# Kernel optimization log

Hardware: AMD Instinct MI355X
Metric: run time of the kernel (lower is better)

## Reference

```python
import jax, jax.numpy as jnp
import numpy as np

HIDDEN_DIM = 512
N = 2 * HIDDEN_DIM  # 1024
B, T_K = 32, 2048


def setup_inputs() -> dict:
    key = jax.random.key(0)
    ks = jax.random.split(key, 10)
    s_t_hat = jax.random.normal(ks[0], (B, N), dtype=jnp.float32)
    encoder_outputs = jax.random.normal(ks[1], (B, T_K, N), dtype=jnp.float32)
    encoder_feature = jax.random.normal(ks[2], (B * T_K, N), dtype=jnp.float32)
    stmt_feature = jax.random.uniform(ks[3], (B, T_K), dtype=jnp.float32) * 0.01
    enc_padding_mask = jnp.ones((B, T_K), dtype=jnp.float32)
    coverage = jax.random.uniform(ks[4], (B, T_K), dtype=jnp.float32)
    # learned params
    W_dec = jax.random.normal(ks[5], (N, N), dtype=jnp.float32) / np.sqrt(N)
    b_dec = jnp.zeros((N,), dtype=jnp.float32)
    v_w = jax.random.normal(ks[6], (N,), dtype=jnp.float32) / np.sqrt(N)
    W_c = jax.random.normal(ks[7], (N,), dtype=jnp.float32)  # Linear(1, N, bias=False)
    return {
        "s_t_hat": s_t_hat,
        "encoder_outputs": encoder_outputs,
        "encoder_feature": encoder_feature,
        "stmt_feature": stmt_feature,
        "enc_padding_mask": enc_padding_mask,
        "coverage": coverage,
        "W_dec": W_dec,
        "b_dec": b_dec,
        "v_w": v_w,
        "W_c": W_c,
    }


def reference(s_t_hat, encoder_outputs, encoder_feature, stmt_feature,
              enc_padding_mask, coverage, W_dec, b_dec, v_w, W_c):
    b, t_k, n = encoder_outputs.shape
    # decode_proj: [b, n]
    dec_fea = s_t_hat @ W_dec.T + b_dec
    # broadcast-add decoder feature + coverage feature (Linear(1, n) == outer product)
    att_features = (encoder_feature.reshape(b, t_k, n)
                    + dec_fea[:, None, :]
                    + coverage[:, :, None] * W_c)  # [b, t_k, n]
    e = jnp.tanh(att_features)
    scores = jnp.einsum('btn,n->bt', e, v_w)  # v: Linear(n, 1, bias=False)
    attn_dist_ = jax.nn.softmax(scores, axis=1) * enc_padding_mask
    attn_dist = attn_dist_ / attn_dist_.sum(axis=1, keepdims=True)
    attn_dist = attn_dist + stmt_feature * enc_padding_mask
    c_t = jnp.einsum('bt,btn->bn', attn_dist, encoder_outputs)  # bmm
    coverage_out = coverage + attn_dist
    return (c_t, attn_dist, coverage_out)
```

## Files before the change

### kernel.cpp

```cpp
#include <hip/hip_runtime.h>

#define B   32
#define TK  2048
#define N   1024
#define NF4 256

#define OUT_CT   0
#define OUT_ATTN (B * N)
#define OUT_COV  (B * N + B * TK)

#define NSLICE 32
#define TPS    (TK / NSLICE)

typedef float v4f __attribute__((ext_vector_type(4)));

__device__ __forceinline__ float hw_exp2(float x) {
    return __builtin_amdgcn_exp2f(x);
}

__device__ __forceinline__ float fast_tanh(float x) {
    float t = hw_exp2(x * 2.8853900817779268f);
    return 1.0f - 2.0f * __builtin_amdgcn_rcpf(t + 1.0f);
}

__device__ __forceinline__ float wave_reduce_sum(float v) {
#pragma unroll
    for (int off = 32; off > 0; off >>= 1) v += __shfl_xor(v, off, 64);
    return v;
}

__device__ __forceinline__ float4 ldnt(const float4* p) {
    v4f v = __builtin_nontemporal_load((const v4f*)p);
    return make_float4(v.x, v.y, v.z, v.w);
}

__global__ __launch_bounds__(256) void decfea_kernel(
    const float4* __restrict__ S,
    const float4* __restrict__ W,
    const float*  __restrict__ bias,
    float*        __restrict__ dec)
{
    int w    = blockIdx.x * 4 + (threadIdx.x >> 6);
    int lane = threadIdx.x & 63;
    int n    = w >> 3;
    int b0   = (w & 7) * 4;

    float4 wr[4];
#pragma unroll
    for (int j = 0; j < 4; ++j) wr[j] = W[n * NF4 + j * 64 + lane];

#pragma unroll
    for (int i = 0; i < 4; ++i) {
        int b = b0 + i;
        float acc = 0.0f;
#pragma unroll
        for (int j = 0; j < 4; ++j) {
            float4 s4 = S[b * NF4 + j * 64 + lane];
            acc += s4.x * wr[j].x + s4.y * wr[j].y + s4.z * wr[j].z + s4.w * wr[j].w;
        }
        acc = wave_reduce_sum(acc);
        if (lane == 0) dec[b * N + n] = acc + bias[n];
    }
}

__global__ __launch_bounds__(256) void scores_kernel(
    const float4* __restrict__ EF,
    const float4* __restrict__ DEC,
    const float4* __restrict__ WC,
    const float4* __restrict__ VW,
    const float*  __restrict__ cov,
    float*        __restrict__ scores)
{
    int w    = blockIdx.x * 4 + (threadIdx.x >> 6);
    int lane = threadIdx.x & 63;
    int r0   = w * 2;
    int b    = r0 >> 11;
    float c0 = cov[r0];
    float c1 = cov[r0 + 1];

    const float4* ef0 = EF + (size_t)r0 * NF4;
    const float4* ef1 = ef0 + NF4;
    const float4* de  = DEC + b * NF4;

    float p0 = 0.0f, p1 = 0.0f;
#pragma unroll
    for (int j = 0; j < 4; ++j) {
        int f = j * 64 + lane;
        float4 e0 = ldnt(ef0 + f);
        float4 e1 = ldnt(ef1 + f);
        float4 d  = de[f];
        float4 wc = WC[f];
        float4 vw = VW[f];
        p0 += fast_tanh(e0.x + d.x + c0 * wc.x) * vw.x;
        p0 += fast_tanh(e0.y + d.y + c0 * wc.y) * vw.y;
        p0 += fast_tanh(e0.z + d.z + c0 * wc.z) * vw.z;
        p0 += fast_tanh(e0.w + d.w + c0 * wc.w) * vw.w;
        p1 += fast_tanh(e1.x + d.x + c1 * wc.x) * vw.x;
        p1 += fast_tanh(e1.y + d.y + c1 * wc.y) * vw.y;
        p1 += fast_tanh(e1.z + d.z + c1 * wc.z) * vw.z;
        p1 += fast_tanh(e1.w + d.w + c1 * wc.w) * vw.w;
    }
    p0 = wave_reduce_sum(p0);
    p1 = wave_reduce_sum(p1);
    if (lane == 0) {
        scores[r0]     = p0;
        scores[r0 + 1] = p1;
    }
}

__global__ __launch_bounds__(256) void softmax_kernel(
    const float* __restrict__ scores,
    const float* __restrict__ mask,
    const float* __restrict__ stmt,
    const float* __restrict__ coverage,
    float*       __restrict__ out)
{
    int b = blockIdx.x, tid = threadIdx.x;
    __shared__ float red[256];

    float s[8];
    float m = -1e30f;
#pragma unroll
    for (int k = 0; k < 8; ++k) {
        s[k] = scores[b * TK + k * 256 + tid];
        m = fmaxf(m, s[k]);
    }
    red[tid] = m;
    __syncthreads();
    for (int step = 128; step > 0; step >>= 1) {
        if (tid < step) red[tid] = fmaxf(red[tid], red[tid + step]);
        __syncthreads();
    }
    float M = red[0];
    __syncthreads();

    float e[8];
    float loc = 0.0f;
#pragma unroll
    for (int k = 0; k < 8; ++k) {
        int t = k * 256 + tid;
        e[k] = hw_exp2((s[k] - M) * 1.4426950408889634f) * mask[b * TK + t];
        loc += e[k];
    }
    red[tid] = loc;
    __syncthreads();
    for (int step = 128; step > 0; step >>= 1) {
        if (tid < step) red[tid] += red[tid + step];
        __syncthreads();
    }
    float inv = 1.0f / red[0];

#pragma unroll
    for (int k = 0; k < 8; ++k) {
        int t = k * 256 + tid;
        int r = b * TK + t;
        float a = e[k] * inv + stmt[r] * mask[r];
        out[OUT_ATTN + r] = a;
        out[OUT_COV + r]  = coverage[r] + a;
    }
}

__global__ __launch_bounds__(256) void ct_partial_kernel(
    const float4* __restrict__ EO,
    const float*  __restrict__ attn,
    float4*       __restrict__ part)
{
    int s = blockIdx.x;
    int b = blockIdx.y;
    int tid = threadIdx.x;

    __shared__ float wbuf[TPS];
    if (tid < TPS) wbuf[tid] = attn[b * TK + s * TPS + tid];
    __syncthreads();

    float4 acc = {0.0f, 0.0f, 0.0f, 0.0f};
    const float4* eo = EO + ((size_t)b * TK + s * TPS) * NF4 + tid;
#pragma unroll 8
    for (int tt = 0; tt < TPS; ++tt) {
        float w  = wbuf[tt];
        float4 v = ldnt(eo + (size_t)tt * NF4);
        acc.x += w * v.x;
        acc.y += w * v.y;
        acc.z += w * v.z;
        acc.w += w * v.w;
    }
    part[((size_t)s * B + b) * NF4 + tid] = acc;
}

__global__ __launch_bounds__(256) void ct_reduce_kernel(
    const float4* __restrict__ part,
    float4*       __restrict__ ct)
{
    int i = blockIdx.x * 256 + threadIdx.x;
    float4 acc = {0.0f, 0.0f, 0.0f, 0.0f};
#pragma unroll
    for (int s = 0; s < NSLICE; ++s) {
        float4 v = part[(size_t)s * (B * NF4) + i];
        acc.x += v.x;
        acc.y += v.y;
        acc.z += v.z;
        acc.w += v.w;
    }
    ct[i] = acc;
}

extern "C" void kernel_launch(void* const* d_in, const int* in_sizes, int n_in,
                              void* d_out, int out_size, void* d_ws, size_t ws_size,
                              hipStream_t stream) {
    const float* s_t_hat = (const float*)d_in[0];
    const float* EO      = (const float*)d_in[1];
    const float* EF      = (const float*)d_in[2];
    const float* stmt    = (const float*)d_in[3];
    const float* mask    = (const float*)d_in[4];
    const float* cov     = (const float*)d_in[5];
    const float* Wdec    = (const float*)d_in[6];
    const float* bdec    = (const float*)d_in[7];
    const float* vw      = (const float*)d_in[8];
    const float* wc      = (const float*)d_in[9];

    float* out = (float*)d_out;
    float* ws  = (float*)d_ws;
    float* dec    = ws;
    float* scores = ws + B * N;
    float* part   = ws + B * N + B * TK;

    decfea_kernel<<<2048, 256, 0, stream>>>(
        (const float4*)s_t_hat, (const float4*)Wdec, bdec, dec);

    scores_kernel<<<8192, 256, 0, stream>>>(
        (const float4*)EF, (const float4*)dec, (const float4*)wc,
        (const float4*)vw, cov, scores);

    softmax_kernel<<<B, 256, 0, stream>>>(scores, mask, stmt, cov, out);

    ct_partial_kernel<<<dim3(NSLICE, B), 256, 0, stream>>>(
        (const float4*)EO, out + OUT_ATTN, (float4*)part);

    ct_reduce_kernel<<<32, 256, 0, stream>>>(
        (const float4*)part, (float4*)(out + OUT_CT));
}
```

Measured before the change: 506.5 us.

## Fuse softmax into context kernel, split c_t by feature slice, widen scores rows

Removes the separate softmax and c_t reduce kernels. Each context block now recomputes the per-batch softmax redundantly and owns a 32-float feature slice across all 2048 timesteps, reducing within the block through shared memory instead of writing and re-reading a partial-sum buffer. The scores kernel now processes four rows per wave instead of two. The trade-offs are that softmax work is repeated 32 times per batch, and encoder_outputs reads are now short strided 128-byte segments per row rather than full contiguous rows.

After: 518.2 us. +2.3%, slower.

```diff
diff --git a/kernel.cpp b/kernel.cpp
--- a/kernel.cpp
+++ b/kernel.cpp
@@ -9,8 +9,8 @@
 #define OUT_ATTN (B * N)
 #define OUT_COV  (B * N + B * TK)
 
-#define NSLICE 32
-#define TPS    (TK / NSLICE)
+#define NS   32
+#define SF4  (NF4 / NS)
 
 typedef float v4f __attribute__((ext_vector_type(4)));
 
@@ -73,21 +73,21 @@
 {
     int w    = blockIdx.x * 4 + (threadIdx.x >> 6);
     int lane = threadIdx.x & 63;
-    int r0   = w * 2;
+    int r0   = w * 4;
     int b    = r0 >> 11;
-    float c0 = cov[r0];
-    float c1 = cov[r0 + 1];
-
-    const float4* ef0 = EF + (size_t)r0 * NF4;
-    const float4* ef1 = ef0 + NF4;
-    const float4* de  = DEC + b * NF4;
-
-    float p0 = 0.0f, p1 = 0.0f;
+    float c0 = cov[r0], c1 = cov[r0 + 1], c2 = cov[r0 + 2], c3 = cov[r0 + 3];
+
+    const float4* ef = EF + (size_t)r0 * NF4;
+    const float4* de = DEC + b * NF4;
+
+    float p0 = 0.0f, p1 = 0.0f, p2 = 0.0f, p3 = 0.0f;
 #pragma unroll
     for (int j = 0; j < 4; ++j) {
         int f = j * 64 + lane;
-        float4 e0 = ldnt(ef0 + f);
-        float4 e1 = ldnt(ef1 + f);
+        float4 e0 = ldnt(ef + f);
+        float4 e1 = ldnt(ef + NF4 + f);
+        float4 e2 = ldnt(ef + 2 * NF4 + f);
+        float4 e3 = ldnt(ef + 3 * NF4 + f);
         float4 d  = de[f];
         float4 wc = WC[f];
         float4 vw = VW[f];
@@ -99,31 +99,45 @@
         p1 += fast_tanh(e1.y + d.y + c1 * wc.y) * vw.y;
         p1 += fast_tanh(e1.z + d.z + c1 * wc.z) * vw.z;
         p1 += fast_tanh(e1.w + d.w + c1 * wc.w) * vw.w;
+        p2 += fast_tanh(e2.x + d.x + c2 * wc.x) * vw.x;
+        p2 += fast_tanh(e2.y + d.y + c2 * wc.y) * vw.y;
+        p2 += fast_tanh(e2.z + d.z + c2 * wc.z) * vw.z;
+        p2 += fast_tanh(e2.w + d.w + c2 * wc.w) * vw.w;
+        p3 += fast_tanh(e3.x + d.x + c3 * wc.x) * vw.x;
+        p3 += fast_tanh(e3.y + d.y + c3 * wc.y) * vw.y;
+        p3 += fast_tanh(e3.z + d.z + c3 * wc.z) * vw.z;
+        p3 += fast_tanh(e3.w + d.w + c3 * wc.w) * vw.w;
     }
     p0 = wave_reduce_sum(p0);
     p1 = wave_reduce_sum(p1);
+    p2 = wave_reduce_sum(p2);
+    p3 = wave_reduce_sum(p3);
     if (lane == 0) {
-        scores[r0]     = p0;
-        scores[r0 + 1] = p1;
-    }
-}
-
-__global__ __launch_bounds__(256) void softmax_kernel(
-    const float* __restrict__ scores,
-    const float* __restrict__ mask,
-    const float* __restrict__ stmt,
-    const float* __restrict__ coverage,
-    float*       __restrict__ out)
+        *(float4*)(scores + r0) = make_float4(p0, p1, p2, p3);
+    }
+}
+
+__global__ __launch_bounds__(256) void ct_fused_kernel(
+    const float4* __restrict__ EO,
+    const float*  __restrict__ scores,
+    const float*  __restrict__ mask,
+    const float*  __restrict__ stmt,
+    const float*  __restrict__ coverage,
+    float*        __restrict__ out)
 {
-    int b = blockIdx.x, tid = threadIdx.x;
+    int s   = blockIdx.x;
+    int b   = blockIdx.y;
+    int tid = threadIdx.x;
+
+    __shared__ __align__(16) float attn_s[TK];
     __shared__ float red[256];
 
-    float s[8];
+    float sc[8];
     float m = -1e30f;
 #pragma unroll
     for (int k = 0; k < 8; ++k) {
-        s[k] = scores[b * TK + k * 256 + tid];
-        m = fmaxf(m, s[k]);
+        sc[k] = scores[b * TK + k * 256 + tid];
+        m = fmaxf(m, sc[k]);
     }
     red[tid] = m;
     __syncthreads();
@@ -139,7 +153,7 @@
 #pragma unroll
     for (int k = 0; k < 8; ++k) {
         int t = k * 256 + tid;
-        e[k] = hw_exp2((s[k] - M) * 1.4426950408889634f) * mask[b * TK + t];
+        e[k] = hw_exp2((sc[k] - M) * 1.4426950408889634f) * mask[b * TK + t];
         loc += e[k];
     }
     red[tid] = loc;
@@ -155,53 +169,41 @@
         int t = k * 256 + tid;
         int r = b * TK + t;
         float a = e[k] * inv + stmt[r] * mask[r];
-        out[OUT_ATTN + r] = a;
-        out[OUT_COV + r]  = coverage[r] + a;
-    }
-}
-
-__global__ __launch_bounds__(256) void ct_partial_kernel(
-    const float4* __restrict__ EO,
-    const float*  __restrict__ attn,
-    float4*       __restrict__ part)
-{
-    int s = blockIdx.x;
-    int b = blockIdx.y;
-    int tid = threadIdx.x;
-
-    __shared__ float wbuf[TPS];
-    if (tid < TPS) wbuf[tid] = attn[b * TK + s * TPS + tid];
-    __syncthreads();
-
+        attn_s[t] = a;
+        if (s == 0) {
+            out[OUT_ATTN + r] = a;
+            out[OUT_COV + r]  = coverage[r] + a;
+        }
+    }
+    __syncthreads();
+
+    int f = tid & 7;
+    int c = tid >> 3;
     float4 acc = {0.0f, 0.0f, 0.0f, 0.0f};
-    const float4* eo = EO + ((size_t)b * TK + s * TPS) * NF4 + tid;
+    const float4* eo = EO + ((size_t)b * TK + c) * NF4 + s * SF4 + f;
 #pragma unroll 8
-    for (int tt = 0; tt < TPS; ++tt) {
-        float w  = wbuf[tt];
-        float4 v = ldnt(eo + (size_t)tt * NF4);
-        acc.x += w * v.x;
-        acc.y += w * v.y;
-        acc.z += w * v.z;
-        acc.w += w * v.w;
-    }
-    part[((size_t)s * B + b) * NF4 + tid] = acc;
-}
-
-__global__ __launch_bounds__(256) void ct_reduce_kernel(
-    const float4* __restrict__ part,
-    float4*       __restrict__ ct)
-{
-    int i = blockIdx.x * 256 + threadIdx.x;
-    float4 acc = {0.0f, 0.0f, 0.0f, 0.0f};
-#pragma unroll
-    for (int s = 0; s < NSLICE; ++s) {
-        float4 v = part[(size_t)s * (B * NF4) + i];
-        acc.x += v.x;
-        acc.y += v.y;
-        acc.z += v.z;
-        acc.w += v.w;
-    }
-    ct[i] = acc;
+    for (int i = 0; i < 64; ++i) {
+        float wgt = attn_s[i * 32 + c];
+        float4 v  = ldnt(eo + (size_t)i * 32 * NF4);
+        acc.x += wgt * v.x;
+        acc.y += wgt * v.y;
+        acc.z += wgt * v.z;
+        acc.w += wgt * v.w;
+    }
+    __syncthreads();
+
+    float4* part = (float4*)attn_s;
+    part[tid] = acc;
+    __syncthreads();
+    if (tid < SF4) {
+        float4 sum = {0.0f, 0.0f, 0.0f, 0.0f};
+#pragma unroll
+        for (int cc = 0; cc < 32; ++cc) {
+            float4 v = part[cc * SF4 + tid];
+            sum.x += v.x; sum.y += v.y; sum.z += v.z; sum.w += v.w;
+        }
+        ((float4*)(out + OUT_CT))[b * NF4 + s * SF4 + tid] = sum;
+    }
 }
 
 extern "C" void kernel_launch(void* const* d_in, const int* in_sizes, int n_in,
@@ -222,20 +224,14 @@
     float* ws  = (float*)d_ws;
     float* dec    = ws;
     float* scores = ws + B * N;
-    float* part   = ws + B * N + B * TK;
 
     decfea_kernel<<<2048, 256, 0, stream>>>(
         (const float4*)s_t_hat, (const float4*)Wdec, bdec, dec);
 
-    scores_kernel<<<8192, 256, 0, stream>>>(
+    scores_kernel<<<4096, 256, 0, stream>>>(
         (const float4*)EF, (const float4*)dec, (const float4*)wc,
         (const float4*)vw, cov, scores);
 
-    softmax_kernel<<<B, 256, 0, stream>>>(scores, mask, stmt, cov, out);
-
-    ct_partial_kernel<<<dim3(NSLICE, B), 256, 0, stream>>>(
-        (const float4*)EO, out + OUT_ATTN, (float4*)part);
-
-    ct_reduce_kernel<<<32, 256, 0, stream>>>(
-        (const float4*)part, (float4*)(out + OUT_CT));
-}
+    ct_fused_kernel<<<dim3(NS, B), 256, 0, stream>>>(
+        (const float4*)EO, scores, mask, stmt, cov, out);
+}
```
